# Performance work log

Measured on AMD Instinct MI355X. Metric: run time of the kernel, lower is better.

## Reference

```python
import jax, jax.numpy as jnp
import numpy as np

N_EMBD = 1024
N_HEAD = 16
B, T = 4, 2048


def setup_inputs() -> dict:
    key = jax.random.key(0)
    ks = jax.random.split(key, 5)
    s_in = 1.0 / np.sqrt(N_EMBD)
    return {
        "x": jax.random.normal(ks[0], (B, T, N_EMBD), dtype=jnp.float32),
        "W_qkv": jax.random.normal(ks[1], (N_EMBD, 3 * N_EMBD), dtype=jnp.float32) * s_in,
        "b_qkv": jnp.zeros((3 * N_EMBD,), dtype=jnp.float32),
        "W_proj": jax.random.normal(ks[2], (N_EMBD, N_EMBD), dtype=jnp.float32) * s_in,
        "b_proj": jnp.zeros((N_EMBD,), dtype=jnp.float32),
    }


def reference(x, W_qkv, b_qkv, W_proj, b_proj):
    Bx, Tx, C = x.shape
    hd = C // N_HEAD
    qkv = x @ W_qkv + b_qkv                      # [B,T,3C]
    q, k, v = jnp.split(qkv, 3, axis=2)

    def rs(t):
        return t.reshape(Bx, Tx, N_HEAD, hd).transpose(0, 2, 1, 3)  # [B,H,T,hd]

    q, k, v = rs(q), rs(k), rs(v)
    scale = 1.0 / np.sqrt(hd)
    attn = jnp.einsum('bhqd,bhkd->bhqk', q, k) * scale
    causal = jnp.tril(jnp.ones((Tx, Tx), dtype=bool))
    attn = jnp.where(causal[None, None], attn, -jnp.inf)
    attn = jax.nn.softmax(attn, axis=-1)
    out = jnp.einsum('bhqk,bhkd->bhqd', attn, v)
    out = out.transpose(0, 2, 1, 3).reshape(Bx, Tx, C)
    return out @ W_proj + b_proj
```

## Files before the change

kernel.cpp:

```cpp
#include <hip/hip_runtime.h>
#include <hip/hip_bf16.h>

typedef __attribute__((ext_vector_type(8))) short short8;
typedef __attribute__((ext_vector_type(4))) float f32x4;

#define QSCALE 0.1803368801111204f

__device__ inline unsigned short f2b(float f){
  union { float f; unsigned int u; } a; a.f = f;
  unsigned int u = a.u;
  unsigned int r = (u + 0x7fff + ((u >> 16) & 1)) >> 16;
  return (unsigned short)r;
}

__device__ inline unsigned short f2brn(float f){
  __hip_bfloat16 h = __float2bfloat16(f);
  union { __hip_bfloat16 h; unsigned short u; } c; c.h = h;
  return c.u;
}

__device__ inline void gload16(const unsigned short* g, unsigned short* l){
  __builtin_amdgcn_global_load_lds((const __attribute__((address_space(1))) void*)g,
                                   (__attribute__((address_space(3))) void*)l, 16, 0, 0);
}

__device__ inline unsigned long long shfl64(unsigned long long v, int src){
  int lo = __shfl((int)(unsigned)(v & 0xffffffffull), src);
  int hi = __shfl((int)(unsigned)(v >> 32), src);
  return ((unsigned long long)(unsigned)hi << 32) | (unsigned)(unsigned int)lo;
}

__global__ void k_cast_x(const float* __restrict__ x, unsigned short* __restrict__ xb, int n4){
  int i = blockIdx.x * blockDim.x + threadIdx.x;
  if (i < n4){
    float4 v = ((const float4*)x)[i];
    ushort4 o;
    o.x = f2b(v.x); o.y = f2b(v.y); o.z = f2b(v.z); o.w = f2b(v.w);
    ((ushort4*)xb)[i] = o;
  }
}

__global__ void k_transpose_cast(const float* __restrict__ in, unsigned short* __restrict__ out,
                                 int R, int Cc){
  __shared__ float tile[32][33];
  int bx = blockIdx.x, by = blockIdx.y;
  int tx = threadIdx.x, ty = threadIdx.y;
  int col = bx*32 + tx;
  #pragma unroll
  for (int jj = 0; jj < 4; ++jj){
    int row = by*32 + ty + jj*8;
    tile[ty + jj*8][tx] = in[(size_t)row*Cc + col];
  }
  __syncthreads();
  int r = by*32 + tx;
  #pragma unroll
  for (int jj = 0; jj < 4; ++jj){
    int c = bx*32 + ty + jj*8;
    out[(size_t)c*R + r] = f2b(tile[tx][ty + jj*8]);
  }
}

template<int MODE>
__global__ __launch_bounds__(256) void k_gemm_bt(
    const unsigned short* __restrict__ A,
    const unsigned short* __restrict__ Bt,
    const float* __restrict__ bias,
    float* __restrict__ Cout,
    unsigned short* __restrict__ qb,
    unsigned short* __restrict__ kbf,
    unsigned short* __restrict__ vbf,
    int Mdim, int Ndim, int Kdim)
{
  __shared__ alignas(16) unsigned short As[3*128*32];
  __shared__ alignas(16) unsigned short Bs[3*128*32];
  const int tid  = threadIdx.x;
  const int lane = tid & 63;
  const int wid  = tid >> 6;
  const int wm   = wid >> 1, wn = wid & 1;
  const int bn   = blockIdx.x, bm = blockIdx.y;
  const int l15  = lane & 15, lhi = lane >> 4;

  f32x4 acc[4][4] = {};

  const int rowA0 = bm * 128, rowB0 = bn * 128;
  const unsigned short* Ag = A  + (size_t)(rowA0 + (tid>>2)) * Kdim + (tid&3)*8;
  const unsigned short* Bg = Bt + (size_t)(rowB0 + (tid>>2)) * Kdim + (tid&3)*8;
  const size_t row64 = (size_t)64 * Kdim;

  const int nK = Kdim >> 5;

#define G_STAGE(t, b) do {                                   \
    const int _ko = (t)*32;                                  \
    unsigned short* _as = As + (b)*4096;                     \
    unsigned short* _bs = Bs + (b)*4096;                     \
    gload16(Ag + _ko,         _as + tid*8);                  \
    gload16(Ag + row64 + _ko, _as + 2048 + tid*8);           \
    gload16(Bg + _ko,         _bs + tid*8);                  \
    gload16(Bg + row64 + _ko, _bs + 2048 + tid*8);           \
  } while(0)

  G_STAGE(0, 0);
  G_STAGE(1, 1);

  int cb = 0, sb = 2;
  for (int kt = 0; kt < nK; ++kt){
    if (kt + 1 < nK) { asm volatile("s_waitcnt vmcnt(4)" ::: "memory"); }
    else             { asm volatile("s_waitcnt vmcnt(0)" ::: "memory"); }
    __builtin_amdgcn_s_barrier();
    if (kt + 2 < nK) G_STAGE(kt + 2, sb);
    const unsigned short* Ac = As + cb*4096;
    const unsigned short* Bc = Bs + cb*4096;
    short8 af[4], bfr[4];
    #pragma unroll
    for (int f = 0; f < 4; ++f){
      af[f]  = *(const short8*)(Ac + (wm*64 + f*16 + l15)*32 + lhi*8);
      bfr[f] = *(const short8*)(Bc + (wn*64 + f*16 + l15)*32 + lhi*8);
    }
    __builtin_amdgcn_s_setprio(1);
    #pragma unroll
    for (int fm = 0; fm < 4; ++fm)
      #pragma unroll
      for (int fn = 0; fn < 4; ++fn)
        acc[fm][fn] = __builtin_amdgcn_mfma_f32_16x16x32_bf16(af[fm], bfr[fn], acc[fm][fn], 0, 0, 0);
    __builtin_amdgcn_s_setprio(0);
    cb = (cb == 2) ? 0 : cb + 1;
    sb = (sb == 2) ? 0 : sb + 1;
  }
#undef G_STAGE

  #pragma unroll
  for (int fm = 0; fm < 4; ++fm){
    #pragma unroll
    for (int fn = 0; fn < 4; ++fn){
      int n  = bn*128 + wn*64 + fn*16 + l15;
      int m0 = bm*128 + wm*64 + fm*16 + lhi*4;
      if (MODE == 0){
        int which = n >> 10; int cc2 = n & 1023; int h = cc2 >> 6; int d = cc2 & 63;
        int bb = m0 >> 11;   int t0 = m0 & 2047;
        if (which == 2){
          float bv = bias[n];
          unsigned long long pk = 0;
          #pragma unroll
          for (int j = 0; j < 4; ++j)
            pk |= (unsigned long long)f2b(acc[fm][fn][j] + bv) << (16*j);
          *(unsigned long long*)(vbf + ((size_t)(bb*16 + h)*64 + d)*2048 + t0) = pk;
        } else {
          unsigned short* dst = (which == 0) ? qb : kbf;
          float bv = bias[n];
          #pragma unroll
          for (int j = 0; j < 4; ++j){
            float v = acc[fm][fn][j] + bv;
            if (which == 0) v *= QSCALE;
            dst[(size_t)((bb*16 + h)*2048 + t0 + j)*64 + d] = f2b(v);
          }
        }
      } else {
        float bv = bias[n];
        #pragma unroll
        for (int j = 0; j < 4; ++j)
          Cout[(size_t)(m0 + j) * Ndim + n] = acc[fm][fn][j] + bv;
      }
    }
  }
}

__global__ __launch_bounds__(256) void k_attn(
    const unsigned short* __restrict__ qb,
    const unsigned short* __restrict__ kbuf,
    const unsigned short* __restrict__ vT,
    unsigned short* __restrict__ ao)
{
  __shared__ alignas(16) unsigned short K_lds[2*64*64];
  __shared__ alignas(16) unsigned short V_lds[2*64*64];
  const int tid  = threadIdx.x;
  const int lane = tid & 63, wid = tid >> 6;
  const int l15  = lane & 15, lhi = lane >> 4;
  const int qt   = (int)gridDim.x - 1 - (int)blockIdx.x;
  const int bh   = blockIdx.y;
  const size_t base = (size_t)bh * 2048 * 64;
  const int q0w  = qt*128 + wid*32;
  const int qmaxw = q0w + 31;

  const int sr  = tid >> 3;
  const int sck = (tid & 7) ^ (sr & 7);
  const unsigned short* kg0 = kbuf + base + (size_t)(sr     )*64 + sck*8;
  const unsigned short* kg1 = kbuf + base + (size_t)(sr + 32)*64 + sck*8;
  const unsigned short* vg0 = vT   + base + (size_t)(sr     )*2048 + sck*8;
  const unsigned short* vg1 = vT   + base + (size_t)(sr + 32)*2048 + sck*8;

#define A_STAGE(t, b) do {                                   \
    const int _kb = (t)*64;                                  \
    unsigned short* _kd = K_lds + (b)*4096;                  \
    unsigned short* _vd = V_lds + (b)*4096;                  \
    gload16(kg0 + (size_t)_kb*64, _kd + tid*8);              \
    gload16(kg1 + (size_t)_kb*64, _kd + 2048 + tid*8);       \
    gload16(vg0 + _kb,            _vd + tid*8);              \
    gload16(vg1 + _kb,            _vd + 2048 + tid*8);       \
  } while(0)

  short8 qf[2][2];
  #pragma unroll
  for (int g = 0; g < 2; ++g)
    #pragma unroll
    for (int i = 0; i < 2; ++i)
      qf[g][i] = *(const short8*)(qb + base + (size_t)(q0w + g*16 + l15)*64 + i*32 + lhi*8);

  float m_run[2] = {-1e30f, -1e30f};
  float l_run[2] = {0.f, 0.f};
  f32x4 o_acc[2][4] = {};

  const int nkt = 2*qt + 2;

  const int bs = ((lhi & 1) << 1) | (lhi >> 1);
  const int sA = l15 + (bs << 4);
  const int sB = l15 + ((bs ^ 1) << 4);
  const bool selodd = (lhi & 1);
  const bool lowh   = (lhi < 2);

  A_STAGE(0, 0);

  for (int kt = 0; kt < nkt; ++kt){
    if (kt + 1 < nkt){
      A_STAGE(kt + 1, (kt + 1) & 1);
      asm volatile("s_waitcnt vmcnt(4)" ::: "memory");
    } else {
      asm volatile("s_waitcnt vmcnt(0)" ::: "memory");
    }
    __builtin_amdgcn_s_barrier();
    if (kt*64 <= qmaxw){
      const unsigned short* Kc = K_lds + (kt & 1)*4096;
      const unsigned short* Vc = V_lds + (kt & 1)*4096;
      short8 kf[4][2];
      #pragma unroll
      for (int fn = 0; fn < 4; ++fn)
        #pragma unroll
        for (int i = 0; i < 2; ++i)
          kf[fn][i] = *(const short8*)(Kc + (fn*16 + l15)*64 + (((i*4 + lhi) ^ (l15 & 7)) << 3));
      f32x4 s[2][4] = {};
      __builtin_amdgcn_s_setprio(1);
      #pragma unroll
      for (int g = 0; g < 2; ++g)
        #pragma unroll
        for (int fn = 0; fn < 4; ++fn)
          #pragma unroll
          for (int i = 0; i < 2; ++i)
            s[g][fn] = __builtin_amdgcn_mfma_f32_16x16x32_bf16(kf[fn][i], qf[g][i], s[g][fn], 0, 0, 0);
      __builtin_amdgcn_s_setprio(0);
      if (kt >= 2*qt){
        #pragma unroll
        for (int g = 0; g < 2; ++g){
          const int qi = q0w + g*16 + l15;
          #pragma unroll
          for (int fn = 0; fn < 4; ++fn)
            #pragma unroll
            for (int j = 0; j < 4; ++j){
              int ki = kt*64 + fn*16 + lhi*4 + j;
              if (ki > qi) s[g][fn][j] = -1e30f;
            }
        }
      }
      float rmax[2];
      #pragma unroll
      for (int g = 0; g < 2; ++g){
        float t0 = fmaxf(fmaxf(s[g][0][0], s[g][0][1]), fmaxf(s[g][0][2], s[g][0][3]));
        float t1 = fmaxf(fmaxf(s[g][1][0], s[g][1][1]), fmaxf(s[g][1][2], s[g][1][3]));
        float t2 = fmaxf(fmaxf(s[g][2][0], s[g][2][1]), fmaxf(s[g][2][2], s[g][2][3]));
        float t3 = fmaxf(fmaxf(s[g][3][0], s[g][3][1]), fmaxf(s[g][3][2], s[g][3][3]));
        float v = fmaxf(fmaxf(t0, t1), fmaxf(t2, t3));
        v = fmaxf(v, __shfl_xor(v, 16));
        v = fmaxf(v, __shfl_xor(v, 32));
        rmax[g] = v;
      }
      bool need = (rmax[0] > m_run[0] + 8.f) || (rmax[1] > m_run[1] + 8.f);
      if (__any(need)){
        #pragma unroll
        for (int g = 0; g < 2; ++g){
          float mn   = fmaxf(m_run[g], rmax[g]);
          float corr = exp2f(m_run[g] - mn);
          m_run[g] = mn;
          l_run[g] *= corr;
          #pragma unroll
          for (int j = 0; j < 4; ++j){
            float cj = __shfl(corr, (lane & 48) | (lhi*4 + j));
            #pragma unroll
            for (int df = 0; df < 4; ++df) o_acc[g][df][j] *= cj;
          }
        }
      }
      unsigned long long pwq[2][4];
      #pragma unroll
      for (int g = 0; g < 2; ++g){
        const float mr = m_run[g];
        float rsum = 0.f;
        #pragma unroll
        for (int fn = 0; fn < 4; ++fn){
          float e0 = exp2f(s[g][fn][0] - mr);
          float e1 = exp2f(s[g][fn][1] - mr);
          float e2 = exp2f(s[g][fn][2] - mr);
          float e3 = exp2f(s[g][fn][3] - mr);
          rsum += (e0 + e1) + (e2 + e3);
          unsigned int w0 = (unsigned int)f2brn(e0) | ((unsigned int)f2brn(e1) << 16);
          unsigned int w1 = (unsigned int)f2brn(e2) | ((unsigned int)f2brn(e3) << 16);
          pwq[g][fn] = (unsigned long long)w0 | ((unsigned long long)w1 << 32);
        }
        rsum += __shfl_xor(rsum, 16);
        rsum += __shfl_xor(rsum, 32);
        l_run[g] += rsum;
      }
      short8 pa[2][2];
      #pragma unroll
      for (int g = 0; g < 2; ++g){
        unsigned long long pubA0 = selodd ? pwq[g][1] : pwq[g][0];
        unsigned long long pubB0 = selodd ? pwq[g][0] : pwq[g][1];
        unsigned long long pubA1 = selodd ? pwq[g][3] : pwq[g][2];
        unsigned long long pubB1 = selodd ? pwq[g][2] : pwq[g][3];
        unsigned long long rA0 = shfl64(pubA0, sA);
        unsigned long long rB0 = shfl64(pubB0, sB);
        unsigned long long rA1 = shfl64(pubA1, sA);
        unsigned long long rB1 = shfl64(pubB1, sB);
        union { unsigned long long q[2]; short8 v; } u0, u1;
        u0.q[0] = lowh ? rA0 : rB0;  u0.q[1] = lowh ? rB0 : rA0;
        u1.q[0] = lowh ? rA1 : rB1;  u1.q[1] = lowh ? rB1 : rA1;
        pa[g][0] = u0.v;  pa[g][1] = u1.v;
      }
      __builtin_amdgcn_s_setprio(1);
      #pragma unroll
      for (int df = 0; df < 4; ++df){
        #pragma unroll
        for (int i = 0; i < 2; ++i){
          short8 vf = *(const short8*)(Vc + (df*16 + l15)*64 + (((i*4 + lhi) ^ (l15 & 7)) << 3));
          #pragma unroll
          for (int g = 0; g < 2; ++g)
            o_acc[g][df] = __builtin_amdgcn_mfma_f32_16x16x32_bf16(pa[g][i], vf, o_acc[g][df], 0, 0, 0);
        }
      }
      __builtin_amdgcn_s_setprio(0);
    }
    __builtin_amdgcn_s_barrier();
  }
#undef A_STAGE
  const int b = bh >> 4, h = bh & 15;
  #pragma unroll
  for (int g = 0; g < 2; ++g){
    float rln = 1.0f / l_run[g];
    #pragma unroll
    for (int j = 0; j < 4; ++j){
      float rl = __shfl(rln, (lane & 48) | (lhi*4 + j));
      int qrow = q0w + g*16 + lhi*4 + j;
      #pragma unroll
      for (int df = 0; df < 4; ++df){
        float v = o_acc[g][df][j] * rl;
        ao[(size_t)(b*2048 + qrow)*1024 + h*64 + df*16 + l15] = f2brn(v);
      }
    }
  }
}

extern "C" void kernel_launch(void* const* d_in, const int* in_sizes, int n_in,
                              void* d_out, int out_size, void* d_ws, size_t ws_size,
                              hipStream_t stream){
  const float* x     = (const float*)d_in[0];
  const float* Wqkv  = (const float*)d_in[1];
  const float* bqkv  = (const float*)d_in[2];
  const float* Wproj = (const float*)d_in[3];
  const float* bproj = (const float*)d_in[4];
  float* out = (float*)d_out;

  unsigned short* ws     = (unsigned short*)d_ws;
  unsigned short* xb     = ws;
  unsigned short* wqkvT  = xb + 8388608;
  unsigned short* wprojT = wqkvT + 3145728;
  unsigned short* qbuf   = wprojT + 1048576;
  unsigned short* kbuf   = qbuf + 8388608;
  unsigned short* vbuf   = kbuf + 8388608;
  unsigned short* ao     = vbuf + 8388608;

  k_cast_x<<<8192, 256, 0, stream>>>(x, xb, 2097152);
  k_transpose_cast<<<dim3(96, 32), dim3(32, 8), 0, stream>>>(Wqkv, wqkvT, 1024, 3072);
  k_transpose_cast<<<dim3(32, 32), dim3(32, 8), 0, stream>>>(Wproj, wprojT, 1024, 1024);
  k_gemm_bt<0><<<dim3(24, 64), 256, 0, stream>>>(xb, wqkvT, bqkv, nullptr,
                                                 qbuf, kbuf, vbuf, 8192, 3072, 1024);
  k_attn<<<dim3(16, 64), 256, 0, stream>>>(qbuf, kbuf, vbuf, ao);
  k_gemm_bt<1><<<dim3(8, 64), 256, 0, stream>>>(ao, wprojT, bproj, out,
                                                nullptr, nullptr, nullptr, 8192, 1024, 1024);
}
```

Before: 368.5 us.

## Switch attention kernel to 32x32x16 MFMA with permlane32 swap for P

Rewrites the attention inner loop to use 32x32x16 bf16 MFMA instead of 16x16x32. Each lane now owns one query row, so the row max and row sum need a single cross-half shuffle and the rescale no longer has to shuffle correction factors. The P fragments are rearranged for the PV matmul with v_permlane32_swap instead of 64-bit shuffles. The output is written with 8-byte packed stores. The larger f32x16 accumulators raise register pressure, and the permlane lane mapping must match the MFMA operand layout exactly.

```diff
diff --git a/kernel.cpp b/kernel.cpp
--- a/kernel.cpp
+++ b/kernel.cpp
@@ -3,6 +3,7 @@
 
 typedef __attribute__((ext_vector_type(8))) short short8;
 typedef __attribute__((ext_vector_type(4))) float f32x4;
+typedef __attribute__((ext_vector_type(16))) float f32x16;
 
 #define QSCALE 0.1803368801111204f
 
@@ -18,16 +19,13 @@
   union { __hip_bfloat16 h; unsigned short u; } c; c.h = h;
   return c.u;
 }
+__device__ inline unsigned pk2(float lo, float hi){
+  return (unsigned)f2brn(lo) | ((unsigned)f2brn(hi) << 16);
+}
 
 __device__ inline void gload16(const unsigned short* g, unsigned short* l){
   __builtin_amdgcn_global_load_lds((const __attribute__((address_space(1))) void*)g,
                                    (__attribute__((address_space(3))) void*)l, 16, 0, 0);
-}
-
-__device__ inline unsigned long long shfl64(unsigned long long v, int src){
-  int lo = __shfl((int)(unsigned)(v & 0xffffffffull), src);
-  int hi = __shfl((int)(unsigned)(v >> 32), src);
-  return ((unsigned long long)(unsigned)hi << 32) | (unsigned)(unsigned int)lo;
 }
 
 __global__ void k_cast_x(const float* __restrict__ x, unsigned short* __restrict__ xb, int n4){
@@ -174,12 +172,13 @@
   __shared__ alignas(16) unsigned short V_lds[2*64*64];
   const int tid  = threadIdx.x;
   const int lane = tid & 63, wid = tid >> 6;
-  const int l15  = lane & 15, lhi = lane >> 4;
+  const int l31  = lane & 31, h = lane >> 5;
   const int qt   = (int)gridDim.x - 1 - (int)blockIdx.x;
   const int bh   = blockIdx.y;
   const size_t base = (size_t)bh * 2048 * 64;
   const int q0w  = qt*128 + wid*32;
   const int qmaxw = q0w + 31;
+  const int myq  = q0w + l31;
 
   const int sr  = tid >> 3;
   const int sck = (tid & 7) ^ (sr & 7);
@@ -198,24 +197,16 @@
     gload16(vg1 + _kb,            _vd + 2048 + tid*8);       \
   } while(0)
 
-  short8 qf[2][2];
-  #pragma unroll
-  for (int g = 0; g < 2; ++g)
-    #pragma unroll
-    for (int i = 0; i < 2; ++i)
-      qf[g][i] = *(const short8*)(qb + base + (size_t)(q0w + g*16 + l15)*64 + i*32 + lhi*8);
-
-  float m_run[2] = {-1e30f, -1e30f};
-  float l_run[2] = {0.f, 0.f};
-  f32x4 o_acc[2][4] = {};
+  short8 qf[4];
+  #pragma unroll
+  for (int c = 0; c < 4; ++c)
+    qf[c] = *(const short8*)(qb + base + (size_t)myq*64 + c*16 + h*8);
+
+  float m_run = -1e30f, l_run = 0.f;
+  f32x16 oa0 = {}, oa1 = {};
 
   const int nkt = 2*qt + 2;
-
-  const int bs = ((lhi & 1) << 1) | (lhi >> 1);
-  const int sA = l15 + (bs << 4);
-  const int sB = l15 + ((bs ^ 1) << 4);
-  const bool selodd = (lhi & 1);
-  const bool lowh   = (lhi < 2);
+  const int swr = (l31 & 7);
 
   A_STAGE(0, 0);
 
@@ -230,129 +221,111 @@
     if (kt*64 <= qmaxw){
       const unsigned short* Kc = K_lds + (kt & 1)*4096;
       const unsigned short* Vc = V_lds + (kt & 1)*4096;
-      short8 kf[4][2];
-      #pragma unroll
-      for (int fn = 0; fn < 4; ++fn)
-        #pragma unroll
-        for (int i = 0; i < 2; ++i)
-          kf[fn][i] = *(const short8*)(Kc + (fn*16 + l15)*64 + (((i*4 + lhi) ^ (l15 & 7)) << 3));
-      f32x4 s[2][4] = {};
+      short8 kf0[4], kf1[4];
+      #pragma unroll
+      for (int c = 0; c < 4; ++c){
+        const int ch = ((2*c + h) ^ swr) << 3;
+        kf0[c] = *(const short8*)(Kc + (l31     )*64 + ch);
+        kf1[c] = *(const short8*)(Kc + (l31 + 32)*64 + ch);
+      }
+      f32x16 s0 = {}, s1 = {};
       __builtin_amdgcn_s_setprio(1);
       #pragma unroll
-      for (int g = 0; g < 2; ++g)
-        #pragma unroll
-        for (int fn = 0; fn < 4; ++fn)
-          #pragma unroll
-          for (int i = 0; i < 2; ++i)
-            s[g][fn] = __builtin_amdgcn_mfma_f32_16x16x32_bf16(kf[fn][i], qf[g][i], s[g][fn], 0, 0, 0);
+      for (int c = 0; c < 4; ++c)
+        s0 = __builtin_amdgcn_mfma_f32_32x32x16_bf16(kf0[c], qf[c], s0, 0, 0, 0);
+      #pragma unroll
+      for (int c = 0; c < 4; ++c)
+        s1 = __builtin_amdgcn_mfma_f32_32x32x16_bf16(kf1[c], qf[c], s1, 0, 0, 0);
       __builtin_amdgcn_s_setprio(0);
       if (kt >= 2*qt){
+        const int kb0 = kt*64 + 4*h;
         #pragma unroll
-        for (int g = 0; g < 2; ++g){
-          const int qi = q0w + g*16 + l15;
-          #pragma unroll
-          for (int fn = 0; fn < 4; ++fn)
-            #pragma unroll
-            for (int j = 0; j < 4; ++j){
-              int ki = kt*64 + fn*16 + lhi*4 + j;
-              if (ki > qi) s[g][fn][j] = -1e30f;
-            }
+        for (int r = 0; r < 16; ++r){
+          int k0 = kb0 + (r & 3) + 8*(r >> 2);
+          if (k0      > myq) s0[r] = -1e30f;
+          if (k0 + 32 > myq) s1[r] = -1e30f;
         }
       }
-      float rmax[2];
-      #pragma unroll
-      for (int g = 0; g < 2; ++g){
-        float t0 = fmaxf(fmaxf(s[g][0][0], s[g][0][1]), fmaxf(s[g][0][2], s[g][0][3]));
-        float t1 = fmaxf(fmaxf(s[g][1][0], s[g][1][1]), fmaxf(s[g][1][2], s[g][1][3]));
-        float t2 = fmaxf(fmaxf(s[g][2][0], s[g][2][1]), fmaxf(s[g][2][2], s[g][2][3]));
-        float t3 = fmaxf(fmaxf(s[g][3][0], s[g][3][1]), fmaxf(s[g][3][2], s[g][3][3]));
-        float v = fmaxf(fmaxf(t0, t1), fmaxf(t2, t3));
-        v = fmaxf(v, __shfl_xor(v, 16));
-        v = fmaxf(v, __shfl_xor(v, 32));
-        rmax[g] = v;
-      }
-      bool need = (rmax[0] > m_run[0] + 8.f) || (rmax[1] > m_run[1] + 8.f);
-      if (__any(need)){
+      float ma = -1e30f, mb = -1e30f, mc = -1e30f, md = -1e30f;
+      #pragma unroll
+      for (int r = 0; r < 16; r += 4){
+        ma = fmaxf(ma, fmaxf(s0[r],   s0[r+1]));
+        mb = fmaxf(mb, fmaxf(s0[r+2], s0[r+3]));
+        mc = fmaxf(mc, fmaxf(s1[r],   s1[r+1]));
+        md = fmaxf(md, fmaxf(s1[r+2], s1[r+3]));
+      }
+      float rmax = fmaxf(fmaxf(ma, mb), fmaxf(mc, md));
+      rmax = fmaxf(rmax, __shfl_xor(rmax, 32));
+      if (__any(rmax > m_run + 8.f)){
+        float mn   = fmaxf(m_run, rmax);
+        float corr = exp2f(m_run - mn);
+        m_run = mn;
+        l_run *= corr;
         #pragma unroll
-        for (int g = 0; g < 2; ++g){
-          float mn   = fmaxf(m_run[g], rmax[g]);
-          float corr = exp2f(m_run[g] - mn);
-          m_run[g] = mn;
-          l_run[g] *= corr;
-          #pragma unroll
-          for (int j = 0; j < 4; ++j){
-            float cj = __shfl(corr, (lane & 48) | (lhi*4 + j));
-            #pragma unroll
-            for (int df = 0; df < 4; ++df) o_acc[g][df][j] *= cj;
-          }
+        for (int r = 0; r < 16; ++r){ oa0[r] *= corr; oa1[r] *= corr; }
+      }
+      unsigned w0q[8], w1q[8];
+      float rsa = 0.f, rsb = 0.f;
+      #pragma unroll
+      for (int m = 0; m < 4; ++m){
+        float a0 = exp2f(s0[4*m]   - m_run), a1 = exp2f(s0[4*m+1] - m_run);
+        float a2 = exp2f(s0[4*m+2] - m_run), a3 = exp2f(s0[4*m+3] - m_run);
+        float b0 = exp2f(s1[4*m]   - m_run), b1 = exp2f(s1[4*m+1] - m_run);
+        float b2 = exp2f(s1[4*m+2] - m_run), b3 = exp2f(s1[4*m+3] - m_run);
+        rsa += (a0 + a1) + (a2 + a3);
+        rsb += (b0 + b1) + (b2 + b3);
+        w0q[2*m] = pk2(a0, a1); w0q[2*m+1] = pk2(a2, a3);
+        w1q[2*m] = pk2(b0, b1); w1q[2*m+1] = pk2(b2, b3);
+      }
+      float rsum = rsa + rsb;
+      rsum += __shfl_xor(rsum, 32);
+      l_run += rsum;
+      short8 pa[4];
+      #pragma unroll
+      for (int cc = 0; cc < 2; ++cc){
+        {
+          unsigned x0 = w0q[4*cc], x1 = w0q[4*cc+1], y0 = w0q[4*cc+2], y1 = w0q[4*cc+3];
+          asm("v_permlane32_swap_b32 %0, %1" : "+v"(x0), "+v"(y0));
+          asm("v_permlane32_swap_b32 %0, %1" : "+v"(x1), "+v"(y1));
+          union { unsigned u[4]; short8 v; } t; t.u[0]=x0; t.u[1]=x1; t.u[2]=y0; t.u[3]=y1;
+          pa[cc] = t.v;
         }
-      }
-      unsigned long long pwq[2][4];
-      #pragma unroll
-      for (int g = 0; g < 2; ++g){
-        const float mr = m_run[g];
-        float rsum = 0.f;
-        #pragma unroll
-        for (int fn = 0; fn < 4; ++fn){
-          float e0 = exp2f(s[g][fn][0] - mr);
-          float e1 = exp2f(s[g][fn][1] - mr);
-          float e2 = exp2f(s[g][fn][2] - mr);
-          float e3 = exp2f(s[g][fn][3] - mr);
-          rsum += (e0 + e1) + (e2 + e3);
-          unsigned int w0 = (unsigned int)f2brn(e0) | ((unsigned int)f2brn(e1) << 16);
-          unsigned int w1 = (unsigned int)f2brn(e2) | ((unsigned int)f2brn(e3) << 16);
-          pwq[g][fn] = (unsigned long long)w0 | ((unsigned long long)w1 << 32);
+        {
+          unsigned x0 = w1q[4*cc], x1 = w1q[4*cc+1], y0 = w1q[4*cc+2], y1 = w1q[4*cc+3];
+          asm("v_permlane32_swap_b32 %0, %1" : "+v"(x0), "+v"(y0));
+          asm("v_permlane32_swap_b32 %0, %1" : "+v"(x1), "+v"(y1));
+          union { unsigned u[4]; short8 v; } t; t.u[0]=x0; t.u[1]=x1; t.u[2]=y0; t.u[3]=y1;
+          pa[2+cc] = t.v;
         }
-        rsum += __shfl_xor(rsum, 16);
-        rsum += __shfl_xor(rsum, 32);
-        l_run[g] += rsum;
-      }
-      short8 pa[2][2];
-      #pragma unroll
-      for (int g = 0; g < 2; ++g){
-        unsigned long long pubA0 = selodd ? pwq[g][1] : pwq[g][0];
-        unsigned long long pubB0 = selodd ? pwq[g][0] : pwq[g][1];
-        unsigned long long pubA1 = selodd ? pwq[g][3] : pwq[g][2];
-        unsigned long long pubB1 = selodd ? pwq[g][2] : pwq[g][3];
-        unsigned long long rA0 = shfl64(pubA0, sA);
-        unsigned long long rB0 = shfl64(pubB0, sB);
-        unsigned long long rA1 = shfl64(pubA1, sA);
-        unsigned long long rB1 = shfl64(pubB1, sB);
-        union { unsigned long long q[2]; short8 v; } u0, u1;
-        u0.q[0] = lowh ? rA0 : rB0;  u0.q[1] = lowh ? rB0 : rA0;
-        u1.q[0] = lowh ? rA1 : rB1;  u1.q[1] = lowh ? rB1 : rA1;
-        pa[g][0] = u0.v;  pa[g][1] = u1.v;
       }
       __builtin_amdgcn_s_setprio(1);
       #pragma unroll
-      for (int df = 0; df < 4; ++df){
-        #pragma unroll
-        for (int i = 0; i < 2; ++i){
-          short8 vf = *(const short8*)(Vc + (df*16 + l15)*64 + (((i*4 + lhi) ^ (l15 & 7)) << 3));
-          #pragma unroll
-          for (int g = 0; g < 2; ++g)
-            o_acc[g][df] = __builtin_amdgcn_mfma_f32_16x16x32_bf16(pa[g][i], vf, o_acc[g][df], 0, 0, 0);
-        }
+      for (int c = 0; c < 4; ++c){
+        const int ch = ((2*c + h) ^ swr) << 3;
+        short8 vf0 = *(const short8*)(Vc + (l31     )*64 + ch);
+        short8 vf1 = *(const short8*)(Vc + (l31 + 32)*64 + ch);
+        oa0 = __builtin_amdgcn_mfma_f32_32x32x16_bf16(vf0, pa[c], oa0, 0, 0, 0);
+        oa1 = __builtin_amdgcn_mfma_f32_32x32x16_bf16(vf1, pa[c], oa1, 0, 0, 0);
       }
       __builtin_amdgcn_s_setprio(0);
     }
     __builtin_amdgcn_s_barrier();
   }
 #undef A_STAGE
-  const int b = bh >> 4, h = bh & 15;
-  #pragma unroll
-  for (int g = 0; g < 2; ++g){
-    float rln = 1.0f / l_run[g];
+  const int b = bh >> 4, hh = bh & 15;
+  const float rl = 1.0f / l_run;
+  unsigned short* aop = ao + (size_t)(b*2048 + myq)*1024 + hh*64;
+  #pragma unroll
+  for (int rg = 0; rg < 4; ++rg){
+    const int d0 = 8*rg + 4*h;
+    unsigned long long p0 = 0, p1 = 0;
     #pragma unroll
     for (int j = 0; j < 4; ++j){
-      float rl = __shfl(rln, (lane & 48) | (lhi*4 + j));
-      int qrow = q0w + g*16 + lhi*4 + j;
-      #pragma unroll
-      for (int df = 0; df < 4; ++df){
-        float v = o_acc[g][df][j] * rl;
-        ao[(size_t)(b*2048 + qrow)*1024 + h*64 + df*16 + l15] = f2brn(v);
-      }
-    }
+      p0 |= (unsigned long long)f2brn(oa0[4*rg + j] * rl) << (16*j);
+      p1 |= (unsigned long long)f2brn(oa1[4*rg + j] * rl) << (16*j);
+    }
+    *(unsigned long long*)(aop + d0)      = p0;
+    *(unsigned long long*)(aop + 32 + d0) = p1;
   }
 }
 
```

Measured after the change: 353.4 us. -4.1%, faster.
